# Optimization experiments

Hardware: AMD Instinct MI355X
Metric: run time of the kernel (lower is better)

Reference implementation:

```python
import jax, jax.numpy as jnp
import numpy as np

VOCAB = 50000
BATCH = 1024
SEQ = 120
NFEAT = 1
EMBED = 50
HIDDEN = 300
NCLASS = 5
FORGET_BIAS = 1.0  # tf.nn.rnn_cell.LSTMCell default


def setup_inputs() -> dict:
    key = jax.random.key(0)
    k1, k2, k3, k4 = jax.random.split(key, 4)
    input_ids = jax.random.randint(k1, (BATCH, SEQ, NFEAT), 0, VOCAB)
    embeddings = jax.random.normal(k2, (VOCAB, EMBED), jnp.float32)
    # LSTM kernel acts on concat([x, h]) -> 4*H gates (i, j, f, o order, TF convention)
    in_dim = NFEAT * EMBED + HIDDEN
    W_lstm = jax.random.normal(k3, (in_dim, 4 * HIDDEN), jnp.float32) * (1.0 / np.sqrt(in_dim))
    b_lstm = jnp.zeros((4 * HIDDEN,), jnp.float32)
    U = jax.random.normal(k4, (HIDDEN, NCLASS), jnp.float32) * (1.0 / np.sqrt(HIDDEN))
    b2 = jnp.zeros((NCLASS,), jnp.float32)
    return {"input_ids": input_ids, "embeddings": embeddings,
            "W_lstm": W_lstm, "b_lstm": b_lstm, "U": U, "b2": b2}


def reference(input_ids, embeddings, W_lstm, b_lstm, U, b2):
    B, T, F = input_ids.shape
    # embedding lookup + flatten feature dim: (B, T, F*E)
    x = embeddings[input_ids].reshape(B, T, -1)
    H = b_lstm.shape[0] // 4

    def cell(carry, x_t):
        c, h = carry
        z = jnp.concatenate([x_t, h], axis=-1) @ W_lstm + b_lstm  # (B, 4H)
        i, j, f, o = jnp.split(z, 4, axis=-1)  # TF LSTMCell gate order
        c_new = c * jax.nn.sigmoid(f + FORGET_BIAS) + jax.nn.sigmoid(i) * jnp.tanh(j)
        h_new = jnp.tanh(c_new) * jax.nn.sigmoid(o)
        return (c_new, h_new), h_new

    c0 = jnp.zeros((B, H), x.dtype)
    h0 = jnp.zeros((B, H), x.dtype)
    # scan over time; outputs are (T, B, H) which matches the module's final
    # transpose([1,0,2]) of the (B, T, C) preds.
    _, outs = jax.lax.scan(cell, (c0, h0), jnp.swapaxes(x, 0, 1))
    # dropout placeholder is 1.0 at inference -> identity
    preds = outs @ U + b2  # (T, B, n_classes)
    return preds
```

## Files before the change

kernel.cpp:

```cpp
#include <hip/hip_runtime.h>
#include <hip/hip_bf16.h>


#define NB 1024
#define NT 120
#define NE 50
#define NH 300
#define KX 64
#define KH 320
#define KT 384
#define HP 320
#define NGRP 8
#define NCOLB 19
#define ROLES 20
#define GRID 160
#define WCOL_STRIDE 784
#define HSLOTS 4

typedef __bf16 bf16_t;
typedef __bf16 bf16x8 __attribute__((ext_vector_type(8)));
typedef float f32x4 __attribute__((ext_vector_type(4)));

__device__ __forceinline__ float fsig(float x) {
    return __builtin_amdgcn_rcpf(1.0f + __expf(-x));
}
__device__ __forceinline__ float ftanh(float x) {
    return fmaf(2.0f, __builtin_amdgcn_rcpf(1.0f + __expf(-2.0f * x)), -1.0f);
}

__device__ __forceinline__ bf16x8 coh_load8(const bf16_t* p) {
    const unsigned long long* q = (const unsigned long long*)p;
    union { unsigned long long u[2]; bf16x8 v; } t;
    t.u[0] = __hip_atomic_load(q,     __ATOMIC_RELAXED, __HIP_MEMORY_SCOPE_AGENT);
    t.u[1] = __hip_atomic_load(q + 1, __ATOMIC_RELAXED, __HIP_MEMORY_SCOPE_AGENT);
    return t.v;
}
__device__ __forceinline__ void coh_store16(bf16_t* p, bf16_t h) {
    __hip_atomic_store((unsigned short*)p, __builtin_bit_cast(unsigned short, h),
                       __ATOMIC_RELAXED, __HIP_MEMORY_SCOPE_AGENT);
}
__device__ __forceinline__ unsigned coh_loadu(const unsigned* p) {
    return __hip_atomic_load(p, __ATOMIC_RELAXED, __HIP_MEMORY_SCOPE_AGENT);
}

__device__ __forceinline__ void inv_l1() {
    asm volatile("buffer_inv sc0\n\ts_waitcnt vmcnt(0)" ::: "memory");
}
__device__ __forceinline__ unsigned xcc_id() {
    unsigned x;
    asm volatile("s_getreg_b32 %0, hwreg(HW_REG_XCC_ID)" : "=s"(x));
    return x & 0xfu;
}

__global__ void prep_all(const int* __restrict__ ids, const float* __restrict__ emb,
                         const float* __restrict__ W,
                         bf16_t* __restrict__ WpT, uint4* __restrict__ zbase,
                         int nzero, bf16_t* __restrict__ Xp) {
    const long stride = (long)gridDim.x * 256;
    const long g0 = (long)blockIdx.x * 256 + threadIdx.x;

    for (long i = g0; i < nzero; i += stride)
        zbase[i] = make_uint4(0u, 0u, 0u, 0u);

    for (long gid = g0; gid < 4 * HP * KT; gid += stride) {
        int k = (int)(gid % KT);
        int col = (int)(gid / KT);
        int g = col / HP, hc = col % HP;
        int kp = -1;
        if (k < 50) kp = k;
        else if (k >= 64 && k < 364) kp = k - 14;
        float v = 0.0f;
        if (kp >= 0 && hc < NH) v = W[(long)kp * 1200 + g * NH + hc];
        WpT[gid] = (bf16_t)v;
    }

    for (long gid = g0; gid < (long)NB * NT * 4; gid += stride) {
        int s = (int)(gid & 3);
        long bt = gid >> 2;
        int b = (int)(bt / NT), t = (int)(bt % NT);
        int id = ids[bt];
        const float* er = emb + (long)id * NE;
        bf16_t* dst = Xp + ((long)t * NB + b) * KX + s * 16;
#pragma unroll
        for (int j = 0; j < 16; ++j) {
            int e = s * 16 + j;
            dst[j] = (bf16_t)((e < NE) ? er[e] : 0.0f);
        }
    }
}

__global__ void __launch_bounds__(512, 2) lstm_persist(
    const float* __restrict__ bl, const bf16_t* __restrict__ WpT,
    bf16_t* Hbase,
    const bf16_t* __restrict__ Xp,
    unsigned* flgG, unsigned* flgP, unsigned* xcdA,
    const float* __restrict__ U, const float* __restrict__ b2,
    float* __restrict__ out)
{
    __shared__ __align__(16) unsigned char smem[64 * WCOL_STRIDE];
    __shared__ int sLocalOK;
    const int blk = blockIdx.x;
    const int tid = threadIdx.x;
    const int g = blk & 7;
    const int c = blk >> 3;
    const int lane = tid & 63, wave = tid >> 6;

    if (tid == 0)
        __hip_atomic_store(xcdA + blk, xcc_id() + 1u,
                           __ATOMIC_RELAXED, __HIP_MEMORY_SCOPE_AGENT);
    if (wave == 0) {
        unsigned v = 1u;
        for (;;) {
            if (lane < ROLES)
                v = coh_loadu(xcdA + (lane * NGRP + g));
            if (__all(v != 0)) break;
            __builtin_amdgcn_s_sleep(1);
        }
        unsigned ref = __shfl(v, 0, 64);
        int ok = __all(lane >= ROLES || v == ref);
        if (lane == 0) sLocalOK = ok;
    }

    unsigned* gBase = flgG + (long)g * NT * ROLES;
    unsigned* pBase = flgP + (long)g * NT;
    const size_t HSZ = (size_t)NB * KH;

    if (c < NCOLB) {
        for (int ch = tid; ch < 64 * 48; ch += 512) {
            int col = ch / 48, pq = ch % 48;
            int gt = col >> 4, mm = col & 15;
            int hc = c * 16 + mm;
            const uint4* src = (const uint4*)(WpT + (long)(gt * HP + hc) * KT) + pq;
            *(uint4*)(smem + col * WCOL_STRIDE + pq * 16) = *src;
        }

        const int m = lane & 15, quad = lane >> 4;
        const int rbase = g * 128 + wave * 16;
        const int rowA  = rbase + m;
        const int hcOut = c * 16 + m;
        const bool colOK = (hcOut < NH);

        float bias[4] = {0.f, 0.f, 0.f, 0.f};
        if (colOK) {
#pragma unroll
            for (int gt = 0; gt < 4; ++gt) bias[gt] = bl[gt * NH + hcOut];
        }
        float cst[4] = {0.f, 0.f, 0.f, 0.f};

        __syncthreads();
        const bool localOK = (sLocalOK != 0);

        bf16x8 Bh[8][4];
#pragma unroll
        for (int kk = 0; kk < 8; ++kk)
#pragma unroll
            for (int gt = 0; gt < 4; ++gt) {
                Bh[kk][gt] = *(const bf16x8*)(smem + (gt * 16 + m) * WCOL_STRIDE
                                              + ((kk + 2) * 4 + quad) * 16);
                asm volatile("" : "+v"(Bh[kk][gt]));
            }

        for (int t = 0; t < NT; ++t) {
            const bf16x8* xv = (const bf16x8*)(Xp + ((long)t * NB + rowA) * KX);
            bf16x8 ax[2];
#pragma unroll
            for (int kk = 0; kk < 2; ++kk) ax[kk] = xv[kk * 4 + quad];

            f32x4 acc[4];
#pragma unroll
            for (int gt = 0; gt < 4; ++gt) acc[gt] = (f32x4){0.f, 0.f, 0.f, 0.f};
#pragma unroll
            for (int kk = 0; kk < 2; ++kk) {
#pragma unroll
                for (int gt = 0; gt < 4; ++gt) {
                    bf16x8 b = *(const bf16x8*)(smem + (gt * 16 + m) * WCOL_STRIDE
                                                + (kk * 4 + quad) * 16);
                    acc[gt] = __builtin_amdgcn_mfma_f32_16x16x32_bf16(ax[kk], b, acc[gt], 0, 0, 0);
                }
            }

            if (t > 0) {
                if (wave == 0) {
                    const unsigned* gf = gBase + (long)(t - 1) * ROLES;
                    const bool needP = (t >= HSLOTS);
                    const unsigned* ap = (lane < NCOLB) ? (gf + lane)
                                                        : (pBase + (t - HSLOTS));
                    const bool active = (lane < NCOLB) || (lane == NCOLB && needP);
                    if (localOK) {
                        for (;;) {
                            inv_l1();
                            unsigned v = active ? *(const volatile unsigned*)ap : 1u;
                            if (__all(v != 0)) break;
                            __builtin_amdgcn_s_sleep(1);
                        }
                    } else {
                        for (;;) {
                            unsigned v = active ? coh_loadu(ap) : 1u;
                            if (__all(v != 0)) break;
                            __builtin_amdgcn_s_sleep(1);
                        }
                    }
                }
            }
            __syncthreads();
            __builtin_amdgcn_sched_barrier(0);

            const bf16_t* Hr = Hbase + (size_t)((t + 3) & 3) * HSZ;
            bf16_t*       Hw = Hbase + (size_t)(t & 3) * HSZ;

            const bf16_t* hp = Hr + (long)rowA * KH;
            bf16x8 ah[10];
            if (localOK) {
                const bf16x8* hv = (const bf16x8*)hp;
#pragma unroll
                for (int i = 0; i < 10; ++i) ah[i] = hv[i * 4 + quad];
            } else {
#pragma unroll
                for (int i = 0; i < 10; ++i) ah[i] = coh_load8(hp + (i * 4 + quad) * 8);
            }
            __builtin_amdgcn_sched_barrier(0);

#pragma unroll
            for (int kk = 2; kk < 10; ++kk) {
#pragma unroll
                for (int gt = 0; gt < 4; ++gt)
                    acc[gt] = __builtin_amdgcn_mfma_f32_16x16x32_bf16(
                        ah[kk - 2], Bh[kk - 2][gt], acc[gt], 0, 0, 0);
            }
#pragma unroll
            for (int kk = 10; kk < 12; ++kk) {
#pragma unroll
                for (int gt = 0; gt < 4; ++gt) {
                    bf16x8 b = *(const bf16x8*)(smem + (gt * 16 + m) * WCOL_STRIDE
                                                + (kk * 4 + quad) * 16);
                    acc[gt] = __builtin_amdgcn_mfma_f32_16x16x32_bf16(ah[kk - 2], b, acc[gt], 0, 0, 0);
                }
            }

            float hn_[4];
#pragma unroll
            for (int r = 0; r < 4; ++r) {
                float zi = acc[0][r] + bias[0];
                float zj = acc[1][r] + bias[1];
                float zf = acc[2][r] + bias[2];
                float zo = acc[3][r] + bias[3];
                float cn = cst[r] * fsig(zf + 1.0f) + fsig(zi) * ftanh(zj);
                cst[r] = cn;
                hn_[r] = ftanh(cn) * fsig(zo);
            }
            if (colOK) {
                if (localOK) {
#pragma unroll
                    for (int r = 0; r < 4; ++r)
                        Hw[(long)(rbase + quad * 4 + r) * KH + hcOut] = (bf16_t)hn_[r];
                } else {
#pragma unroll
                    for (int r = 0; r < 4; ++r)
                        coh_store16(Hw + (long)(rbase + quad * 4 + r) * KH + hcOut,
                                    (bf16_t)hn_[r]);
                }
            }

            __syncthreads();
            if (tid == 0) {
                unsigned* fp = gBase + (long)t * ROLES + c;
                if (localOK) *(volatile unsigned*)fp = 1u;
                else __hip_atomic_store(fp, 1u, __ATOMIC_RELAXED,
                                        __HIP_MEMORY_SCOPE_AGENT);
            }
        }
    } else {
        bf16_t* UThi = (bf16_t*)smem;
        bf16_t* UTlo = (bf16_t*)(smem + 10240);
        for (int i = tid; i < 16 * 320; i += 512) {
            int n = i / 320, k = i % 320;
            float v = (n < 5 && k < NH) ? U[k * 5 + n] : 0.0f;
            bf16_t hi = (bf16_t)v;
            UThi[i] = hi;
            UTlo[i] = (bf16_t)(v - (float)hi);
        }
        const int m = lane & 15, quad = lane >> 4;
        const float b2v = (m < 5) ? b2[m] : 0.0f;
        __syncthreads();
        const bool localOK = (sLocalOK != 0);

        bf16x8 Bu[10][2];
#pragma unroll
        for (int kk = 0; kk < 10; ++kk) {
            Bu[kk][0] = *(const bf16x8*)(UThi + m * 320 + kk * 32 + quad * 8);
            asm volatile("" : "+v"(Bu[kk][0]));
            Bu[kk][1] = *(const bf16x8*)(UTlo + m * 320 + kk * 32 + quad * 8);
            asm volatile("" : "+v"(Bu[kk][1]));
        }
        const int row0 = g * 128 + wave * 16 + m;

        for (int t = 0; t < NT; ++t) {
            if (wave == 0) {
                const unsigned* gf = gBase + (long)t * ROLES;
                if (localOK) {
                    for (;;) {
                        inv_l1();
                        unsigned v = (lane < NCOLB) ? *(const volatile unsigned*)(gf + lane) : 1u;
                        if (__all(v != 0)) break;
                        __builtin_amdgcn_s_sleep(1);
                    }
                } else {
                    for (;;) {
                        unsigned v = (lane < NCOLB) ? coh_loadu(gf + lane) : 1u;
                        if (__all(v != 0)) break;
                        __builtin_amdgcn_s_sleep(1);
                    }
                }
            }
            __syncthreads();
            __builtin_amdgcn_sched_barrier(0);

            const bf16_t* Hs = Hbase + (size_t)(t & 3) * HSZ;
            const bf16_t* hp = Hs + (long)row0 * KH;
            bf16x8 ah[10];
            if (localOK) {
                const bf16x8* hv = (const bf16x8*)hp;
#pragma unroll
                for (int i = 0; i < 10; ++i) ah[i] = hv[i * 4 + quad];
            } else {
#pragma unroll
                for (int i = 0; i < 10; ++i) ah[i] = coh_load8(hp + (i * 4 + quad) * 8);
            }
            __builtin_amdgcn_sched_barrier(0);

            f32x4 acc = (f32x4){0.f, 0.f, 0.f, 0.f};
#pragma unroll
            for (int kk = 0; kk < 10; ++kk) {
                acc = __builtin_amdgcn_mfma_f32_16x16x32_bf16(ah[kk], Bu[kk][0], acc, 0, 0, 0);
                acc = __builtin_amdgcn_mfma_f32_16x16x32_bf16(ah[kk], Bu[kk][1], acc, 0, 0, 0);
            }

            if (m < 5) {
#pragma unroll
                for (int r = 0; r < 4; ++r) {
                    int row = g * 128 + wave * 16 + quad * 4 + r;
                    out[(long)t * (NB * 5) + row * 5 + m] = acc[r] + b2v;
                }
            }

            __syncthreads();
            if (tid == 0) {
                unsigned* fp = pBase + t;
                if (localOK) *(volatile unsigned*)fp = 1u;
                else __hip_atomic_store(fp, 1u, __ATOMIC_RELAXED,
                                        __HIP_MEMORY_SCOPE_AGENT);
            }
        }
    }
}

extern "C" void kernel_launch(void* const* d_in, const int* in_sizes, int n_in,
                              void* d_out, int out_size, void* d_ws, size_t ws_size,
                              hipStream_t stream) {
    const int* ids   = (const int*)d_in[0];
    const float* emb = (const float*)d_in[1];
    const float* W   = (const float*)d_in[2];
    const float* bl  = (const float*)d_in[3];
    const float* U   = (const float*)d_in[4];
    const float* b2  = (const float*)d_in[5];
    float* out = (float*)d_out;

    char* ws = (char*)d_ws;
    bf16_t*   WpT   = (bf16_t*)ws;
    bf16_t*   Hbase = (bf16_t*)(ws + 983040);
    unsigned* flgG  = (unsigned*)(ws + 3604480);
    unsigned* flgP  = (unsigned*)(ws + 3681280);
    unsigned* xcdA  = (unsigned*)(ws + 3685120);
    bf16_t*   Xp    = (bf16_t*)(ws + 3685760);

    prep_all<<<2048, 256, 0, stream>>>(ids, emb, W, WpT,
                                       (uint4*)(ws + 983040), 168920, Xp);

    void* kargs[] = { (void*)&bl, (void*)&WpT, (void*)&Hbase, (void*)&Xp,
                      (void*)&flgG, (void*)&flgP, (void*)&xcdA,
                      (void*)&U, (void*)&b2, (void*)&out };
    hipError_t err = hipLaunchCooperativeKernel((const void*)lstm_persist,
                                                dim3(GRID), dim3(512), kargs, 0, stream);
    if (err != hipSuccess) {
        lstm_persist<<<GRID, 512, 0, stream>>>(bl, WpT, Hbase, Xp,
                                               flgG, flgP, xcdA, U, b2, out);
    }
}
```

Measured before the change: 643.2 us.

## Replace per-block ready flags with atomic counters and deepen hidden-state ring

Each step's inter-block handshake used to write one flag per column block, and waiters polled 19 flags with an L1 invalidate on every poll. Now each column block atomically increments one counter per group and timestep, and the waiter polls a single word, doing one L1 invalidate only after the wait succeeds. The hidden-state ring buffer grows from 4 to 8 slots, so the recurrence can run further ahead of the output projection blocks. The gate bias is folded into the accumulator initialisation, and the h stores are merged into the activation loop. In exchange, atomic contention lands on one address, and the workspace layout and zero-fill size change.

Result: no change. 641.5 us (-0.3%).

```diff
diff --git a/kernel.cpp b/kernel.cpp
--- a/kernel.cpp
+++ b/kernel.cpp
@@ -15,7 +15,7 @@
 #define ROLES 20
 #define GRID 160
 #define WCOL_STRIDE 784
-#define HSLOTS 4
+#define HSLOTS 8
 
 typedef __bf16 bf16_t;
 typedef __bf16 bf16x8 __attribute__((ext_vector_type(8)));
@@ -41,6 +41,9 @@
 }
 __device__ __forceinline__ unsigned coh_loadu(const unsigned* p) {
     return __hip_atomic_load(p, __ATOMIC_RELAXED, __HIP_MEMORY_SCOPE_AGENT);
+}
+__device__ __forceinline__ void cnt_bump(unsigned* p) {
+    __hip_atomic_fetch_add(p, 1u, __ATOMIC_RELAXED, __HIP_MEMORY_SCOPE_AGENT);
 }
 
 __device__ __forceinline__ void inv_l1() {
@@ -93,7 +96,7 @@
     const float* __restrict__ bl, const bf16_t* __restrict__ WpT,
     bf16_t* Hbase,
     const bf16_t* __restrict__ Xp,
-    unsigned* flgG, unsigned* flgP, unsigned* xcdA,
+    unsigned* gcnt, unsigned* pcnt, unsigned* xcdA,
     const float* __restrict__ U, const float* __restrict__ b2,
     float* __restrict__ out)
 {
@@ -121,8 +124,8 @@
         if (lane == 0) sLocalOK = ok;
     }
 
-    unsigned* gBase = flgG + (long)g * NT * ROLES;
-    unsigned* pBase = flgP + (long)g * NT;
+    unsigned* gC = gcnt + (long)g * NT;
+    unsigned* pC = pcnt + (long)g * NT;
     const size_t HSZ = (size_t)NB * KH;
 
     if (c < NCOLB) {
@@ -168,7 +171,8 @@
 
             f32x4 acc[4];
 #pragma unroll
-            for (int gt = 0; gt < 4; ++gt) acc[gt] = (f32x4){0.f, 0.f, 0.f, 0.f};
+            for (int gt = 0; gt < 4; ++gt)
+                acc[gt] = (f32x4){bias[gt], bias[gt], bias[gt], bias[gt]};
 #pragma unroll
             for (int kk = 0; kk < 2; ++kk) {
 #pragma unroll
@@ -181,32 +185,24 @@
 
             if (t > 0) {
                 if (wave == 0) {
-                    const unsigned* gf = gBase + (long)(t - 1) * ROLES;
+                    unsigned* gcp = gC + (t - 1);
+                    unsigned* pcp = pC + (t - HSLOTS);
                     const bool needP = (t >= HSLOTS);
-                    const unsigned* ap = (lane < NCOLB) ? (gf + lane)
-                                                        : (pBase + (t - HSLOTS));
-                    const bool active = (lane < NCOLB) || (lane == NCOLB && needP);
-                    if (localOK) {
-                        for (;;) {
-                            inv_l1();
-                            unsigned v = active ? *(const volatile unsigned*)ap : 1u;
-                            if (__all(v != 0)) break;
-                            __builtin_amdgcn_s_sleep(1);
-                        }
-                    } else {
-                        for (;;) {
-                            unsigned v = active ? coh_loadu(ap) : 1u;
-                            if (__all(v != 0)) break;
-                            __builtin_amdgcn_s_sleep(1);
-                        }
+                    for (;;) {
+                        unsigned v = 19u;
+                        if (lane == 0)               v = coh_loadu(gcp);
+                        else if (lane == 1 && needP) v = 18u + coh_loadu(pcp);
+                        if (__all(v >= 19u)) break;
+                        __builtin_amdgcn_s_sleep(1);
                     }
+                    if (localOK) inv_l1();
                 }
             }
             __syncthreads();
             __builtin_amdgcn_sched_barrier(0);
 
-            const bf16_t* Hr = Hbase + (size_t)((t + 3) & 3) * HSZ;
-            bf16_t*       Hw = Hbase + (size_t)(t & 3) * HSZ;
+            const bf16_t* Hr = Hbase + (size_t)((t + HSLOTS - 1) & (HSLOTS - 1)) * HSZ;
+            bf16_t*       Hw = Hbase + (size_t)(t & (HSLOTS - 1)) * HSZ;
 
             const bf16_t* hp = Hr + (long)rowA * KH;
             bf16x8 ah[10];
@@ -237,37 +233,24 @@
                 }
             }
 
-            float hn_[4];
 #pragma unroll
             for (int r = 0; r < 4; ++r) {
-                float zi = acc[0][r] + bias[0];
-                float zj = acc[1][r] + bias[1];
-                float zf = acc[2][r] + bias[2];
-                float zo = acc[3][r] + bias[3];
+                float zi = acc[0][r];
+                float zj = acc[1][r];
+                float zf = acc[2][r];
+                float zo = acc[3][r];
                 float cn = cst[r] * fsig(zf + 1.0f) + fsig(zi) * ftanh(zj);
                 cst[r] = cn;
-                hn_[r] = ftanh(cn) * fsig(zo);
-            }
-            if (colOK) {
-                if (localOK) {
-#pragma unroll
-                    for (int r = 0; r < 4; ++r)
-                        Hw[(long)(rbase + quad * 4 + r) * KH + hcOut] = (bf16_t)hn_[r];
-                } else {
-#pragma unroll
-                    for (int r = 0; r < 4; ++r)
-                        coh_store16(Hw + (long)(rbase + quad * 4 + r) * KH + hcOut,
-                                    (bf16_t)hn_[r]);
+                float hn = ftanh(cn) * fsig(zo);
+                if (colOK) {
+                    bf16_t* dst = Hw + (long)(rbase + quad * 4 + r) * KH + hcOut;
+                    if (localOK) *dst = (bf16_t)hn;
+                    else coh_store16(dst, (bf16_t)hn);
                 }
             }
 
             __syncthreads();
-            if (tid == 0) {
-                unsigned* fp = gBase + (long)t * ROLES + c;
-                if (localOK) *(volatile unsigned*)fp = 1u;
-                else __hip_atomic_store(fp, 1u, __ATOMIC_RELAXED,
-                                        __HIP_MEMORY_SCOPE_AGENT);
-            }
+            if (tid == 0) cnt_bump(gC + t);
         }
     } else {
         bf16_t* UThi = (bf16_t*)smem;
@@ -296,26 +279,19 @@
 
         for (int t = 0; t < NT; ++t) {
             if (wave == 0) {
-                const unsigned* gf = gBase + (long)t * ROLES;
-                if (localOK) {
-                    for (;;) {
-                        inv_l1();
-                        unsigned v = (lane < NCOLB) ? *(const volatile unsigned*)(gf + lane) : 1u;
-                        if (__all(v != 0)) break;
-                        __builtin_amdgcn_s_sleep(1);
-                    }
-                } else {
-                    for (;;) {
-                        unsigned v = (lane < NCOLB) ? coh_loadu(gf + lane) : 1u;
-                        if (__all(v != 0)) break;
-                        __builtin_amdgcn_s_sleep(1);
-                    }
-                }
+                unsigned* gcp = gC + t;
+                for (;;) {
+                    unsigned v = 19u;
+                    if (lane == 0) v = coh_loadu(gcp);
+                    if (__all(v >= 19u)) break;
+                    __builtin_amdgcn_s_sleep(1);
+                }
+                if (localOK) inv_l1();
             }
             __syncthreads();
             __builtin_amdgcn_sched_barrier(0);
 
-            const bf16_t* Hs = Hbase + (size_t)(t & 3) * HSZ;
+            const bf16_t* Hs = Hbase + (size_t)(t & (HSLOTS - 1)) * HSZ;
             const bf16_t* hp = Hs + (long)row0 * KH;
             bf16x8 ah[10];
             if (localOK) {
@@ -344,12 +320,7 @@
             }
 
             __syncthreads();
-            if (tid == 0) {
-                unsigned* fp = pBase + t;
-                if (localOK) *(volatile unsigned*)fp = 1u;
-                else __hip_atomic_store(fp, 1u, __ATOMIC_RELAXED,
-                                        __HIP_MEMORY_SCOPE_AGENT);
-            }
+            if (tid == 0) cnt_bump(pC + t);
         }
     }
 }
@@ -368,21 +339,21 @@
     char* ws = (char*)d_ws;
     bf16_t*   WpT   = (bf16_t*)ws;
     bf16_t*   Hbase = (bf16_t*)(ws + 983040);
-    unsigned* flgG  = (unsigned*)(ws + 3604480);
-    unsigned* flgP  = (unsigned*)(ws + 3681280);
-    unsigned* xcdA  = (unsigned*)(ws + 3685120);
-    bf16_t*   Xp    = (bf16_t*)(ws + 3685760);
+    unsigned* gcnt  = (unsigned*)(ws + 6225920);
+    unsigned* pcnt  = (unsigned*)(ws + 6229760);
+    unsigned* xcdA  = (unsigned*)(ws + 6233600);
+    bf16_t*   Xp    = (bf16_t*)(ws + 6234240);
 
     prep_all<<<2048, 256, 0, stream>>>(ids, emb, W, WpT,
-                                       (uint4*)(ws + 983040), 168920, Xp);
+                                       (uint4*)(ws + 983040), 328200, Xp);
 
     void* kargs[] = { (void*)&bl, (void*)&WpT, (void*)&Hbase, (void*)&Xp,
-                      (void*)&flgG, (void*)&flgP, (void*)&xcdA,
+                      (void*)&gcnt, (void*)&pcnt, (void*)&xcdA,
                       (void*)&U, (void*)&b2, (void*)&out };
     hipError_t err = hipLaunchCooperativeKernel((const void*)lstm_persist,
                                                 dim3(GRID), dim3(512), kargs, 0, stream);
     if (err != hipSuccess) {
         lstm_persist<<<GRID, 512, 0, stream>>>(bl, WpT, Hbase, Xp,
-                                               flgG, flgP, xcdA, U, b2, out);
-    }
-}
+                                               gcnt, pcnt, xcdA, U, b2, out);
+    }
+}
```
